# Optimization experiments

Measured on AMD Instinct MI355X. Metric: run time of the kernel, lower is better.

The kernel has to match this reference:

```python
import jax, jax.numpy as jnp
import numpy as np

H = 256      # hidden_dim
L = 3        # nb_layer
N = 10000    # nodes (shared between graph_1 and graph_2)
E1 = 131072  # edges in graph_1
E2 = 65536   # edges in graph_2
B = 16       # number of subgraphs / t_value batch


def _mlp(x, W0, b0, W1, b1, W2, b2):
    h = jax.nn.relu(x @ W0 + b0)
    h = jax.nn.relu(h @ W1 + b1)
    return h @ W2 + b2


def _gatv2(x, src, dst, e, Wl, bl, Wr, br, We, att, bias, n):
    # PyG GATv2Conv (heads=1): gather node features by edge, LeakyReLU attention
    # with edge encodings, scatter-softmax over destination nodes, scatter-add.
    xl = x @ Wl + bl                                            # (N, H)
    xr = x @ Wr + br                                            # (N, H)
    m = jax.nn.leaky_relu(xl[src] + xr[dst] + e @ We, 0.2)      # (E, H)
    logits = m @ att                                            # (E,)
    seg_max = jax.ops.segment_max(logits, dst, num_segments=n)
    ex = jnp.exp(logits - seg_max[dst])
    denom = jax.ops.segment_sum(ex, dst, num_segments=n)
    alpha = ex / (denom[dst] + 1e-16)                           # (E,)
    out = jax.ops.segment_sum(xl[src] * alpha[:, None], dst, num_segments=n)
    return out + bias


def _forward(edge_attr1, edge_attr2, t_value,
             te_W0, te_b0, te_W1, te_b1, te_W2, te_b2,
             ee_W0, ee_b0, ee_W1, ee_b1, ee_W2, ee_b2,
             dec_W0, dec_b0, dec_W1, dec_b1, dec_W2, dec_b2,
             gg_Wl, gg_bl, gg_Wr, gg_br, gg_We, gg_att, gg_bias,
             gf_Wl, gf_bl, gf_Wr, gf_br, gf_We, gf_att, gf_bias,
             edge_index1, edge_index2, batch):
    n = batch.shape[0]
    # time encoding per node, duplicated to 2H node features
    t_enc = _mlp(t_value[batch][:, None], te_W0, te_b0, te_W1, te_b1, te_W2, te_b2)  # (N, H)
    x = jnp.concatenate([t_enc, t_enc], axis=1)                                      # (N, 2H)
    e1 = _mlp(edge_attr1, ee_W0, ee_b0, ee_W1, ee_b1, ee_W2, ee_b2)                  # (E1, H)
    e2 = _mlp(edge_attr2[:, None], ee_W0, ee_b0, ee_W1, ee_b1, ee_W2, ee_b2)         # (E2, H)
    e1_init = e1
    src1, dst1 = edge_index1[0], edge_index1[1]
    src2, dst2 = edge_index2[0], edge_index2[1]
    for i in range(L):
        o1 = _gatv2(x, src1, dst1, e1, gg_Wl[i], gg_bl[i], gg_Wr[i], gg_br[i], gg_We[i], gg_att[i], gg_bias[i], n)
        o2 = _gatv2(x, src2, dst2, e2, gf_Wl[i], gf_bl[i], gf_Wr[i], gf_br[i], gf_We[i], gf_att[i], gf_bias[i], n)
        x = jnp.concatenate([o1, o2], axis=1)                                        # (N, 2H)
    # edge decoder: gather node pairs + initial edge encoding -> MLP
    dec_in = jnp.concatenate([x[src1], x[dst1], e1_init], axis=1)                    # (E1, 5H)
    return _mlp(dec_in, dec_W0, dec_b0, dec_W1, dec_b1, dec_W2, dec_b2)              # (E1, 1)


def setup_inputs() -> dict:
    ks = iter(jax.random.split(jax.random.key(0), 48))
    def nrm(shape, s=0.1):
        return jax.random.normal(next(ks), shape, dtype=jnp.float32) * s
    inp = {}
    inp["edge_index1"] = jax.random.randint(next(ks), (2, E1), 0, N)
    inp["edge_attr1"] = jax.random.uniform(next(ks), (E1, 1), dtype=jnp.float32)
    inp["edge_index2"] = jax.random.randint(next(ks), (2, E2), 0, N)
    inp["edge_attr2"] = jax.random.uniform(next(ks), (E2,), dtype=jnp.float32)
    inp["batch"] = jnp.sort(jax.random.randint(next(ks), (N,), 0, B))
    inp["t_value"] = jax.random.normal(next(ks), (B,), dtype=jnp.float32)
    for p in ["te", "ee"]:
        inp[p + "_W0"] = nrm((1, H)); inp[p + "_b0"] = jnp.zeros((H,), jnp.float32)
        inp[p + "_W1"] = nrm((H, H)); inp[p + "_b1"] = jnp.zeros((H,), jnp.float32)
        inp[p + "_W2"] = nrm((H, H)); inp[p + "_b2"] = jnp.zeros((H,), jnp.float32)
    inp["dec_W0"] = nrm((5 * H, H)); inp["dec_b0"] = jnp.zeros((H,), jnp.float32)
    inp["dec_W1"] = nrm((H, H));     inp["dec_b1"] = jnp.zeros((H,), jnp.float32)
    inp["dec_W2"] = nrm((H, 1));     inp["dec_b2"] = jnp.zeros((1,), jnp.float32)
    for p in ["gg", "gf"]:
        inp[p + "_Wl"] = nrm((L, 2 * H, H)); inp[p + "_bl"] = jnp.zeros((L, H), jnp.float32)
        inp[p + "_Wr"] = nrm((L, 2 * H, H)); inp[p + "_br"] = jnp.zeros((L, H), jnp.float32)
        inp[p + "_We"] = nrm((L, H, H))
        inp[p + "_att"] = nrm((L, H))
        inp[p + "_bias"] = jnp.zeros((L, H), jnp.float32)
    return inp


def reference(edge_index1, edge_attr1, edge_index2, edge_attr2, batch, t_value,
              te_W0, te_b0, te_W1, te_b1, te_W2, te_b2,
              ee_W0, ee_b0, ee_W1, ee_b1, ee_W2, ee_b2,
              dec_W0, dec_b0, dec_W1, dec_b1, dec_W2, dec_b2,
              gg_Wl, gg_bl, gg_Wr, gg_br, gg_We, gg_att, gg_bias,
              gf_Wl, gf_bl, gf_Wr, gf_br, gf_We, gf_att, gf_bias):
    return _forward(edge_attr1, edge_attr2, t_value,
                    te_W0, te_b0, te_W1, te_b1, te_W2, te_b2,
                    ee_W0, ee_b0, ee_W1, ee_b1, ee_W2, ee_b2,
                    dec_W0, dec_b0, dec_W1, dec_b1, dec_W2, dec_b2,
                    gg_Wl, gg_bl, gg_Wr, gg_br, gg_We, gg_att, gg_bias,
                    gf_Wl, gf_bl, gf_Wr, gf_br, gf_We, gf_att, gf_bias,
                    edge_index1, edge_index2, batch)
```

## Files before the change

kernel.cpp:

```cpp
#include <hip/hip_runtime.h>

#define Hd 256
#define NNODE 10000
#define NE1 131072
#define NE2 65536
#define TROWS 4097
#define TLD 1792

typedef __attribute__((ext_vector_type(8))) short bf16x8;
typedef __attribute__((ext_vector_type(4))) float f32x4;

#define MFMA16(a, b, c) __builtin_amdgcn_mfma_f32_16x16x32_bf16((a), (b), (c), 0, 0, 0)

__device__ __forceinline__ float b2f(ushort u) { return __uint_as_float(((unsigned)u) << 16); }
__device__ __forceinline__ ushort f2b(float f) {
  unsigned u = __float_as_uint(f);
  return (ushort)((u + 0x7fffu + ((u >> 16) & 1u)) >> 16);
}

__device__ __forceinline__ unsigned comb2(unsigned a, unsigned b, unsigned t) {
  float alo = __uint_as_float(a << 16), ahi = __uint_as_float(a & 0xffff0000u);
  float blo = __uint_as_float(b << 16), bhi = __uint_as_float(b & 0xffff0000u);
  float tlo = __uint_as_float(t << 16), thi = __uint_as_float(t & 0xffff0000u);
  float zlo = fmaxf(alo + blo + tlo, 0.f);
  float zhi = fmaxf(ahi + bhi + thi, 0.f);
  return ((unsigned)f2b(zhi) << 16) | (unsigned)f2b(zlo);
}


__global__ void time_mlp_k(const float* __restrict__ tval,
                           const float* __restrict__ W0, const float* __restrict__ b0,
                           const float* __restrict__ W1, const float* __restrict__ b1,
                           const float* __restrict__ W2, const float* __restrict__ b2,
                           float* __restrict__ tenc) {
  __shared__ float h0[Hd], h1[Hd];
  int b = blockIdx.x, j = threadIdx.x;
  float t = tval[b];
  h0[j] = fmaxf(t * W0[j] + b0[j], 0.f);
  __syncthreads();
  float a = b1[j];
  for (int k = 0; k < Hd; ++k) a += h0[k] * W1[k * Hd + j];
  h1[j] = fmaxf(a, 0.f);
  __syncthreads();
  float c = b2[j];
  for (int k = 0; k < Hd; ++k) c += h1[k] * W2[k * Hd + j];
  tenc[b * Hd + j] = c;
}

__global__ void build_x0_k(const int* __restrict__ batch, const float* __restrict__ tenc,
                           ushort* __restrict__ x0) {
  int idx = blockIdx.x * 256 + threadIdx.x;
  int n = idx >> 9;
  x0[idx] = f2b(tenc[batch[n] * Hd + (idx & 255)]);
}

__global__ void init_small_k(int* __restrict__ cnt1, int* __restrict__ cur1,
                             int* __restrict__ cnt2, int* __restrict__ cur2,
                             float* __restrict__ zerob, float* __restrict__ biascat,
                             const float* __restrict__ gg_bl, const float* __restrict__ gg_br,
                             const float* __restrict__ gf_bl, const float* __restrict__ gf_br) {
  int i = blockIdx.x * 256 + threadIdx.x;
  if (i < NNODE) { cnt1[i] = 0; cur1[i] = 0; cnt2[i] = 0; cur2[i] = 0; return; }
  i -= NNODE;
  if (i < 512) { zerob[i] = 0.f; return; }
  i -= 512;
  if (i < 6144) {
    int layer = i >> 10, c = i & 1023;
    float v;
    if (c < 256)      v = gg_bl[layer * 256 + c];
    else if (c < 512) v = gg_br[layer * 256 + c - 256];
    else if (c < 768) v = gf_bl[layer * 256 + c - 512];
    else              v = gf_br[layer * 256 + c - 768];
    biascat[layer * 1024 + c] = v;
  }
}

__global__ __launch_bounds__(256) void foldv2_k(
    const float* __restrict__ gg_We, const float* __restrict__ gf_We,
    const float* __restrict__ dec_W0, const float* __restrict__ eeW2,
    const float* __restrict__ eeb2,
    float* __restrict__ Wpart, float* __restrict__ bpart) {
  __shared__ float As[32][68];
  __shared__ float Bt[32][68];
  __shared__ float b2s[32];
  const int tid = threadIdx.x;
  const int bx = blockIdx.x, by = blockIdx.y, bz = blockIdx.z;
  const int y = bx >> 2, n0 = (bx & 3) * 64, k0 = by * 64;
  const int j0 = bz * 32;
  const bool by0 = (by == 0);
  const float* src;
  if (y < 6) src = ((y & 1) == 0 ? gg_We : gf_We) + (size_t)(y >> 1) * 65536;
  else       src = dec_W0 + 1024 * 256;
  if (tid < 32) b2s[tid] = eeb2[j0 + tid];
  {
    int nn = tid & 63, jj0 = tid >> 6;
#pragma unroll
    for (int p = 0; p < 8; ++p)
      As[jj0 + 4 * p][nn] = src[(size_t)(j0 + jj0 + 4 * p) * 256 + n0 + nn];
  }
  {
    int jj = tid & 31, kk0 = tid >> 5;
#pragma unroll
    for (int p = 0; p < 8; ++p)
      Bt[jj][kk0 + 8 * p] = eeW2[(size_t)(k0 + kk0 + 8 * p) * 256 + j0 + jj];
  }
  __syncthreads();
  const int tn = tid & 15, tk = tid >> 4;
  float acc[4][4];
#pragma unroll
  for (int a = 0; a < 4; ++a)
#pragma unroll
    for (int b = 0; b < 4; ++b) acc[a][b] = 0.f;
  float bacc[4] = {0.f, 0.f, 0.f, 0.f};
#pragma unroll 8
  for (int j = 0; j < 32; ++j) {
    float4 av = *(const float4*)&As[j][tn * 4];
    float4 bv = *(const float4*)&Bt[j][tk * 4];
    if (by0) {
      float eb = b2s[j];
      bacc[0] += eb * av.x; bacc[1] += eb * av.y;
      bacc[2] += eb * av.z; bacc[3] += eb * av.w;
    }
    acc[0][0] += av.x * bv.x; acc[0][1] += av.x * bv.y;
    acc[0][2] += av.x * bv.z; acc[0][3] += av.x * bv.w;
    acc[1][0] += av.y * bv.x; acc[1][1] += av.y * bv.y;
    acc[1][2] += av.y * bv.z; acc[1][3] += av.y * bv.w;
    acc[2][0] += av.z * bv.x; acc[2][1] += av.z * bv.y;
    acc[2][2] += av.z * bv.z; acc[2][3] += av.z * bv.w;
    acc[3][0] += av.w * bv.x; acc[3][1] += av.w * bv.y;
    acc[3][2] += av.w * bv.z; acc[3][3] += av.w * bv.w;
  }
  float* wp = Wpart + (size_t)bz * 458752;
#pragma unroll
  for (int a = 0; a < 4; ++a) {
    int n = n0 + tn * 4 + a;
#pragma unroll
    for (int b = 0; b < 4; ++b)
      wp[((size_t)y * 256 + n) * 256 + k0 + tk * 4 + b] = acc[a][b];
  }
  if (tk == 0 && by0) {
#pragma unroll
    for (int a = 0; a < 4; ++a)
      bpart[(size_t)bz * 1792 + y * 256 + n0 + tn * 4 + a] = bacc[a];
  }
}

__global__ __launch_bounds__(256) void foldr_k(
    const float* __restrict__ Wpart, const float* __restrict__ bpart,
    const float* __restrict__ dec_b0,
    ushort* __restrict__ WcatT, float* __restrict__ bcat) {
  int idx = blockIdx.x * 256 + threadIdx.x;
  float s = 0.f;
#pragma unroll
  for (int z = 0; z < 8; ++z) s += Wpart[(size_t)z * 458752 + idx];
  WcatT[idx] = f2b(s);
  if (idx < 1792) {
    float b = 0.f;
#pragma unroll
    for (int z = 0; z < 8; ++z) b += bpart[(size_t)z * 1792 + idx];
    if (idx >= 1536) b += dec_b0[idx - 1536];
    bcat[idx] = b;
  }
}

__global__ void build_h0_k(const float* __restrict__ W0, const float* __restrict__ b0,
                           ushort* __restrict__ h0b) {
  int i = blockIdx.x, j = threadIdx.x;
  float a = (float)i / 4096.f;
  h0b[(size_t)i * 256 + j] = f2b(fmaxf(a * W0[j] + b0[j], 0.f));
}

struct TT { const float* src; ushort* dst; int K; int n_off; int ld; int start; };
struct TransArgs { TT t[24]; };

__global__ void trans_all_k(TransArgs a) {
  int b = blockIdx.x;
  int ti = 0;
  while (ti + 1 < 24 && a.t[ti + 1].start <= b) ++ti;
  TT tk = a.t[ti];
  int lb = b - tk.start;
  int gx = tk.K >> 5;
  int k0 = (lb % gx) * 32, n0 = (lb / gx) * 32;
  __shared__ float t[32][33];
  int tx = threadIdx.x & 31, ty = threadIdx.x >> 5;
#pragma unroll
  for (int p = 0; p < 4; ++p)
    t[ty + 8 * p][tx] = tk.src[(size_t)(k0 + ty + 8 * p) * 256 + n0 + tx];
  __syncthreads();
#pragma unroll
  for (int p = 0; p < 4; ++p)
    tk.dst[(size_t)(tk.n_off + n0 + ty + 8 * p) * tk.ld + k0 + tx] = f2b(t[tx][ty + 8 * p]);
}


__global__ void deg_all_k(const int* __restrict__ dst1, int* __restrict__ cnt1,
                          const int* __restrict__ dst2, int* __restrict__ cnt2) {
  int e = blockIdx.x * 256 + threadIdx.x;
  if (e < NE1) atomicAdd(cnt1 + dst1[e], 1);
  else if (e - NE1 < NE2) atomicAdd(cnt2 + dst2[e - NE1], 1);
}

__global__ void scan_k(const int* __restrict__ cnt1, int* __restrict__ rs1,
                       const int* __restrict__ cnt2, int* __restrict__ rs2) {
  const int g = blockIdx.x;
  const int* cnt = g ? cnt2 : cnt1;
  int* rowstart = g ? rs2 : rs1;
  const int E = g ? NE2 : NE1;
  __shared__ int part[626];
  int t = threadIdx.x;
  if (t < 625) {
    int s = 0;
#pragma unroll
    for (int i = 0; i < 16; ++i) s += cnt[t * 16 + i];
    part[t] = s;
  }
  __syncthreads();
  if (t == 0) {
    int run = 0;
    for (int i = 0; i < 625; ++i) { int v = part[i]; part[i] = run; run += v; }
  }
  __syncthreads();
  if (t < 625) {
    int off = part[t];
#pragma unroll
    for (int i = 0; i < 16; ++i) { rowstart[t * 16 + i] = off; off += cnt[t * 16 + i]; }
  }
  if (t == 0) rowstart[NNODE] = E;
}

__global__ void fill_all_k(const int* __restrict__ dst1, const int* __restrict__ rs1,
                           int* __restrict__ cur1, int* __restrict__ eid1,
                           const int* __restrict__ src1, const float* __restrict__ eattr1,
                           int* __restrict__ srcs1, float* __restrict__ attrs1,
                           int* __restrict__ dsts1,
                           const int* __restrict__ dst2, const int* __restrict__ rs2,
                           int* __restrict__ cur2,
                           const int* __restrict__ src2, const float* __restrict__ eattr2,
                           int* __restrict__ srcs2, float* __restrict__ attrs2) {
  int e = blockIdx.x * 256 + threadIdx.x;
  if (e < NE1) {
    int d = dst1[e];
    int idx = rs1[d] + atomicAdd(cur1 + d, 1);
    eid1[idx] = e;
    srcs1[idx] = src1[e];
    attrs1[idx] = eattr1[e];
    dsts1[idx] = d;
  } else if (e - NE1 < NE2) {
    int e2 = e - NE1;
    int d = dst2[e2];
    int idx = rs2[d] + atomicAdd(cur2 + d, 1);
    srcs2[idx] = src2[e2];
    attrs2[idx] = eattr2[e2];
  }
}

__global__ __launch_bounds__(256) void attagg_k(
    const ushort* __restrict__ T, int tcol1, int tcol2,
    const float* __restrict__ att1, const float* __restrict__ att2,
    const ushort* __restrict__ xlr,
    const int* __restrict__ srcs1, const float* __restrict__ attrs1,
    const int* __restrict__ srcs2, const float* __restrict__ attrs2,
    const int* __restrict__ rs1, const int* __restrict__ rs2,
    const float* __restrict__ bias1, const float* __restrict__ bias2,
    ushort* __restrict__ xnext) {
  __shared__ float att_s[2][256], bias_s[2][256];
  __shared__ float acbuf[2][256];
  __shared__ float mden[2][2];
  const int tid = threadIdx.x;
  att_s[0][tid] = att1[tid];
  att_s[1][tid] = att2[tid];
  bias_s[0][tid] = bias1[tid];
  bias_s[1][tid] = bias2[tid];
  __syncthreads();
  const int wave = tid >> 6, lane = tid & 63;
  const int nloc = wave >> 1, sub = wave & 1;
  const bool g1 = blockIdx.x < (NNODE / 2);
  const int nid = (g1 ? blockIdx.x : blockIdx.x - NNODE / 2) * 2 + nloc;
  const int gi = g1 ? 0 : 1;
  const int* srcs = g1 ? srcs1 : srcs2;
  const float* attrs = g1 ? attrs1 : attrs2;
  const int* rowstart = g1 ? rs1 : rs2;
  const int goff = g1 ? 0 : 512;
  const int colbase = g1 ? 0 : 256;
  const ushort* Tg = T + (g1 ? tcol1 : tcol2);
  const int c = lane * 4;
  ushort4 xr4 = *(const ushort4*)(xlr + (size_t)nid * 1024 + goff + 256 + c);
  const float xr0 = b2f(xr4.x), xr1 = b2f(xr4.y), xr2 = b2f(xr4.z), xr3 = b2f(xr4.w);
  const float a0 = att_s[gi][c], a1 = att_s[gi][c + 1];
  const float a2 = att_s[gi][c + 2], a3 = att_s[gi][c + 3];
  const int s0 = rowstart[nid], s1 = rowstart[nid + 1];
  float m = -1e30f;
  float den = 0.f, ac0 = 0.f, ac1 = 0.f, ac2 = 0.f, ac3 = 0.f;
  {
    int i = s0 + sub;
    if (i < s1) {
      ushort4 xv0, lo0;
      ushort4 xv1 = {0, 0, 0, 0}, lo1 = {0, 0, 0, 0};
      {
        int s = srcs[i];
        int i0 = (int)(attrs[i] * 4096.f + 0.5f);
        i0 = i0 < 0 ? 0 : (i0 > 4096 ? 4096 : i0);
        lo0 = *(const ushort4*)(Tg + (size_t)i0 * TLD + c);
        xv0 = *(const ushort4*)(xlr + (size_t)s * 1024 + goff + c);
      }
      if (i + 2 < s1) {
        int s = srcs[i + 2];
        int i0 = (int)(attrs[i + 2] * 4096.f + 0.5f);
        i0 = i0 < 0 ? 0 : (i0 > 4096 ? 4096 : i0);
        lo1 = *(const ushort4*)(Tg + (size_t)i0 * TLD + c);
        xv1 = *(const ushort4*)(xlr + (size_t)s * 1024 + goff + c);
      }
      for (; i < s1; i += 2) {
        ushort4 xv_c = xv0, lo_c = lo0;
        xv0 = xv1; lo0 = lo1;
        if (i + 4 < s1) {
          int s = srcs[i + 4];
          int i0 = (int)(attrs[i + 4] * 4096.f + 0.5f);
          i0 = i0 < 0 ? 0 : (i0 > 4096 ? 4096 : i0);
          lo1 = *(const ushort4*)(Tg + (size_t)i0 * TLD + c);
          xv1 = *(const ushort4*)(xlr + (size_t)s * 1024 + goff + c);
        }
        float x0 = b2f(xv_c.x), x1 = b2f(xv_c.y), x2 = b2f(xv_c.z), x3 = b2f(xv_c.w);
        float z0 = x0 + xr0 + b2f(lo_c.x);
        float z1 = x1 + xr1 + b2f(lo_c.y);
        float z2 = x2 + xr2 + b2f(lo_c.z);
        float z3 = x3 + xr3 + b2f(lo_c.w);
        z0 = z0 > 0.f ? z0 : 0.2f * z0;
        z1 = z1 > 0.f ? z1 : 0.2f * z1;
        z2 = z2 > 0.f ? z2 : 0.2f * z2;
        z3 = z3 > 0.f ? z3 : 0.2f * z3;
        float p = z0 * a0 + z1 * a1 + z2 * a2 + z3 * a3;
#pragma unroll
        for (int dd = 1; dd < 64; dd <<= 1) p += __shfl_xor(p, dd);
        float mn = fmaxf(m, p);
        float sc = __expf(m - mn);
        float ww = __expf(p - mn);
        den = den * sc + ww;
        ac0 = ac0 * sc + ww * x0;
        ac1 = ac1 * sc + ww * x1;
        ac2 = ac2 * sc + ww * x2;
        ac3 = ac3 * sc + ww * x3;
        m = mn;
      }
    }
  }
  if (sub == 1) {
    acbuf[nloc][c + 0] = ac0;
    acbuf[nloc][c + 1] = ac1;
    acbuf[nloc][c + 2] = ac2;
    acbuf[nloc][c + 3] = ac3;
    if (lane == 0) { mden[nloc][0] = m; mden[nloc][1] = den; }
  }
  __syncthreads();
  if (sub == 0) {
    float m1 = mden[nloc][0], den1 = mden[nloc][1];
    float mn = fmaxf(m, m1);
    float sc0 = __expf(m - mn), sc1 = __expf(m1 - mn);
    float d = den * sc0 + den1 * sc1;
    float A0 = ac0 * sc0 + acbuf[nloc][c + 0] * sc1;
    float A1 = ac1 * sc0 + acbuf[nloc][c + 1] * sc1;
    float A2 = ac2 * sc0 + acbuf[nloc][c + 2] * sc1;
    float A3 = ac3 * sc0 + acbuf[nloc][c + 3] * sc1;
    float inv = 1.f / (d + 1e-16f);
    ushort4 o;
    o.x = f2b(A0 * inv + bias_s[gi][c + 0]);
    o.y = f2b(A1 * inv + bias_s[gi][c + 1]);
    o.z = f2b(A2 * inv + bias_s[gi][c + 2]);
    o.w = f2b(A3 * inv + bias_s[gi][c + 3]);
    *(ushort4*)(xnext + (size_t)nid * 512 + colbase + c) = o;
  }
}

template <bool RELU, bool OBF16>
__global__ __launch_bounds__(256, 2) void mgemm_k(
    const ushort* __restrict__ A, int lda, const ushort* __restrict__ WT, int K,
    const float* __restrict__ bias, void* __restrict__ C, int ldc, int M) {
  __shared__ ushort As[64][40];
  __shared__ ushort Bs[256][40];
  const int tid = threadIdx.x;
  const int wave = tid >> 6, lane = tid & 63;
  const int quad = lane >> 4, l15 = lane & 15;
  const int m0 = blockIdx.x * 64;
  const int ncol0 = blockIdx.y * 256;
  const ushort* WTb = WT + (size_t)ncol0 * K;
  const int arow = tid >> 2, akc = (tid & 3) << 3;
  int am = m0 + arow;
  if (am >= M) am = M - 1;
  f32x4 acc[4][4];
#pragma unroll
  for (int i = 0; i < 4; ++i)
#pragma unroll
    for (int j = 0; j < 4; ++j) acc[i][j] = (f32x4){0.f, 0.f, 0.f, 0.f};
  for (int k0 = 0; k0 < K; k0 += 32) {
    *(uint4*)&As[arow][akc] = *(const uint4*)(A + (size_t)am * lda + k0 + akc);
#pragma unroll
    for (int r = 0; r < 4; ++r) {
      int row = arow + r * 64;
      *(uint4*)&Bs[row][akc] = *(const uint4*)(WTb + (size_t)row * K + k0 + akc);
    }
    __syncthreads();
    bf16x8 bfr[4];
#pragma unroll
    for (int ni = 0; ni < 4; ++ni)
      bfr[ni] = *(const bf16x8*)&Bs[wave * 64 + ni * 16 + l15][quad * 8];
#pragma unroll
    for (int mi = 0; mi < 4; ++mi) {
      bf16x8 af = *(const bf16x8*)&As[mi * 16 + l15][quad * 8];
#pragma unroll
      for (int ni = 0; ni < 4; ++ni) acc[mi][ni] = MFMA16(af, bfr[ni], acc[mi][ni]);
    }
    __syncthreads();
  }
#pragma unroll
  for (int mi = 0; mi < 4; ++mi)
#pragma unroll
    for (int ni = 0; ni < 4; ++ni) {
      int c = ncol0 + wave * 64 + ni * 16 + l15;
      float bv = bias[c];
#pragma unroll
      for (int r = 0; r < 4; ++r) {
        int m = m0 + mi * 16 + quad * 4 + r;
        if (m < M) {
          float v = acc[mi][ni][r] + bv;
          if (RELU) v = fmaxf(v, 0.f);
          if (OBF16) ((ushort*)C)[(size_t)m * ldc + c] = f2b(v);
          else       ((float*)C)[(size_t)m * ldc + c] = v;
        }
      }
    }
}

__global__ __launch_bounds__(256, 4) void dec3_k(
    const float* __restrict__ attrs1, const ushort* __restrict__ T,
    const ushort* __restrict__ Z, const int* __restrict__ eid,
    const int* __restrict__ srcs1, const int* __restrict__ dsts1,
    const ushort* __restrict__ W1T, const float* __restrict__ b1,
    const float* __restrict__ W2, const float* __restrict__ b2,
    float* __restrict__ out) {
  __shared__ __align__(16) ushort h0[64][264];
  float* red = (float*)h0;
  const int tid = threadIdx.x;
  const int wave = tid >> 6, lane = tid & 63;
  const int quad = lane >> 4, l15 = lane & 15;
  const int m0 = blockIdx.x * 64;
  const int arow = tid >> 2;
  {
    int gs = srcs1[m0 + arow], gd = dsts1[m0 + arow];
    int i0 = (int)(attrs1[m0 + arow] * 4096.f + 0.5f);
    i0 = i0 < 0 ? 0 : (i0 > 4096 ? 4096 : i0);
    const int cq = (tid & 3) * 8;
    const ushort* za = Z + (size_t)gs * 512 + cq;
    const ushort* zb = Z + (size_t)gd * 512 + 256 + cq;
    const ushort* tz = T + (size_t)i0 * TLD + 1536 + cq;
    uint4 ra[8], rb[8], rt[8];
#pragma unroll
    for (int s = 0; s < 8; ++s) ra[s] = *(const uint4*)(za + 32 * s);
#pragma unroll
    for (int s = 0; s < 8; ++s) rb[s] = *(const uint4*)(zb + 32 * s);
#pragma unroll
    for (int s = 0; s < 8; ++s) rt[s] = *(const uint4*)(tz + 32 * s);
    __builtin_amdgcn_sched_barrier(0);
#pragma unroll
    for (int s = 0; s < 8; ++s) {
      uint4 o;
      o.x = comb2(ra[s].x, rb[s].x, rt[s].x);
      o.y = comb2(ra[s].y, rb[s].y, rt[s].y);
      o.z = comb2(ra[s].z, rb[s].z, rt[s].z);
      o.w = comb2(ra[s].w, rb[s].w, rt[s].w);
      *(uint4*)&h0[arow][cq + 32 * s] = o;
    }
  }
  __syncthreads();
  f32x4 acc2[4][4];
#pragma unroll
  for (int i = 0; i < 4; ++i)
#pragma unroll
    for (int j = 0; j < 4; ++j) acc2[i][j] = (f32x4){0.f, 0.f, 0.f, 0.f};
  for (int k0 = 0; k0 < 256; k0 += 32) {
    bf16x8 bfr[4];
#pragma unroll
    for (int ni = 0; ni < 4; ++ni)
      bfr[ni] = *(const bf16x8*)(W1T + (size_t)(wave * 64 + ni * 16 + l15) * 256 + k0 + quad * 8);
#pragma unroll
    for (int mi = 0; mi < 4; ++mi) {
      bf16x8 af = *(const bf16x8*)&h0[mi * 16 + l15][k0 + quad * 8];
#pragma unroll
      for (int ni = 0; ni < 4; ++ni) acc2[mi][ni] = MFMA16(af, bfr[ni], acc2[mi][ni]);
    }
  }
  float part[4][4];
#pragma unroll
  for (int mi = 0; mi < 4; ++mi)
#pragma unroll
    for (int r = 0; r < 4; ++r) part[mi][r] = 0.f;
#pragma unroll
  for (int mi = 0; mi < 4; ++mi)
#pragma unroll
    for (int ni = 0; ni < 4; ++ni) {
      int c = wave * 64 + ni * 16 + l15;
      float bv = b1[c], wv = W2[c];
#pragma unroll
      for (int r = 0; r < 4; ++r) {
        float v = fmaxf(acc2[mi][ni][r] + bv, 0.f);
        part[mi][r] += v * wv;
      }
    }
#pragma unroll
  for (int d = 1; d < 16; d <<= 1)
#pragma unroll
    for (int mi = 0; mi < 4; ++mi)
#pragma unroll
      for (int r = 0; r < 4; ++r) part[mi][r] += __shfl_xor(part[mi][r], d);
  __syncthreads();
  if (l15 == 0)
#pragma unroll
    for (int mi = 0; mi < 4; ++mi)
#pragma unroll
      for (int r = 0; r < 4; ++r) red[wave * 64 + mi * 16 + quad * 4 + r] = part[mi][r];
  __syncthreads();
  if (tid < 64) {
    float s = red[tid] + red[64 + tid] + red[128 + tid] + red[192 + tid];
    out[eid[m0 + tid]] = s + b2[0];
  }
}


extern "C" void kernel_launch(void* const* d_in, const int* in_sizes, int n_in,
                              void* d_out, int out_size, void* d_ws, size_t ws_size,
                              hipStream_t stream) {
  const int*   eidx1  = (const int*)d_in[0];
  const float* eattr1 = (const float*)d_in[1];
  const int*   eidx2  = (const int*)d_in[2];
  const float* eattr2 = (const float*)d_in[3];
  const int*   batch  = (const int*)d_in[4];
  const float* tval   = (const float*)d_in[5];
  const float* te_W0 = (const float*)d_in[6];
  const float* te_b0 = (const float*)d_in[7];
  const float* te_W1 = (const float*)d_in[8];
  const float* te_b1 = (const float*)d_in[9];
  const float* te_W2 = (const float*)d_in[10];
  const float* te_b2 = (const float*)d_in[11];
  const float* ee_W0 = (const float*)d_in[12];
  const float* ee_b0 = (const float*)d_in[13];
  const float* ee_W1 = (const float*)d_in[14];
  const float* ee_b1 = (const float*)d_in[15];
  const float* ee_W2 = (const float*)d_in[16];
  const float* ee_b2 = (const float*)d_in[17];
  const float* dec_W0 = (const float*)d_in[18];
  const float* dec_b0 = (const float*)d_in[19];
  const float* dec_W1 = (const float*)d_in[20];
  const float* dec_b1 = (const float*)d_in[21];
  const float* dec_W2 = (const float*)d_in[22];
  const float* dec_b2 = (const float*)d_in[23];
  const float* gg_Wl  = (const float*)d_in[24];
  const float* gg_bl  = (const float*)d_in[25];
  const float* gg_Wr  = (const float*)d_in[26];
  const float* gg_br  = (const float*)d_in[27];
  const float* gg_We  = (const float*)d_in[28];
  const float* gg_att = (const float*)d_in[29];
  const float* gg_bias= (const float*)d_in[30];
  const float* gf_Wl  = (const float*)d_in[31];
  const float* gf_bl  = (const float*)d_in[32];
  const float* gf_Wr  = (const float*)d_in[33];
  const float* gf_br  = (const float*)d_in[34];
  const float* gf_We  = (const float*)d_in[35];
  const float* gf_att = (const float*)d_in[36];
  const float* gf_bias= (const float*)d_in[37];
  (void)in_sizes; (void)n_in; (void)out_size; (void)ws_size;

  const int* src1 = eidx1;
  const int* dst1 = eidx1 + NE1;
  const int* src2 = eidx2;
  const int* dst2 = eidx2 + NE2;

  char* base = (char*)d_ws;
  size_t off = 0;
  auto alloc = [&](size_t bytes) {
    void* p = base + off;
    off += (bytes + 255) & ~(size_t)255;
    return p;
  };
  ushort* x_a    = (ushort*)alloc((size_t)NNODE * 512 * 2);
  ushort* x_b    = (ushort*)alloc((size_t)NNODE * 512 * 2);
  ushort* xlr    = (ushort*)alloc((size_t)NNODE * 1024 * 2);
  ushort* Z      = (ushort*)alloc((size_t)NNODE * 512 * 2);
  ushort* h0b    = (ushort*)alloc((size_t)TROWS * 256 * 2);
  ushort* H1     = (ushort*)alloc((size_t)TROWS * 256 * 2);
  ushort* T      = (ushort*)alloc((size_t)TROWS * TLD * 2);
  ushort* WcatT  = (ushort*)alloc((size_t)7 * 256 * 256 * 2);
  float*  bcat   = (float*)alloc((size_t)TLD * 4);
  float*  tenc   = (float*)alloc((size_t)16 * Hd * 4);
  ushort* decZT  = (ushort*)alloc((size_t)512 * 512 * 2);
  ushort* decW1T = (ushort*)alloc((size_t)256 * 256 * 2);
  ushort* eeW1T  = (ushort*)alloc((size_t)256 * 256 * 2);
  ushort* wlrT   = (ushort*)alloc((size_t)6 * 512 * 512 * 2);
  float*  biascat= (float*)alloc((size_t)6 * 1024 * 4);
  float*  zerob  = (float*)alloc((size_t)512 * 4);
  int* cnt1      = (int*)alloc((size_t)NNODE * 4);
  int* cur1      = (int*)alloc((size_t)NNODE * 4);
  int* rs1       = (int*)alloc((size_t)(NNODE + 1) * 4);
  int* eid1      = (int*)alloc((size_t)NE1 * 4);
  int* srcs1     = (int*)alloc((size_t)NE1 * 4);
  float* attrs1  = (float*)alloc((size_t)NE1 * 4);
  int* dsts1     = (int*)alloc((size_t)NE1 * 4);
  int* cnt2      = (int*)alloc((size_t)NNODE * 4);
  int* cur2      = (int*)alloc((size_t)NNODE * 4);
  int* rs2       = (int*)alloc((size_t)(NNODE + 1) * 4);
  int* srcs2     = (int*)alloc((size_t)NE2 * 4);
  float* attrs2  = (float*)alloc((size_t)NE2 * 4);

  float* Wpart = (float*)T;
  float* bpart = (float*)H1;

  float* out = (float*)d_out;

  init_small_k<<<(NNODE + 512 + 6144 + 255) / 256, 256, 0, stream>>>(
      cnt1, cur1, cnt2, cur2, zerob, biascat, gg_bl, gg_br, gf_bl, gf_br);
  foldv2_k<<<dim3(28, 4, 8), 256, 0, stream>>>(gg_We, gf_We, dec_W0, ee_W2, ee_b2,
                                               Wpart, bpart);
  foldr_k<<<1792, 256, 0, stream>>>(Wpart, bpart, dec_b0, WcatT, bcat);
  build_h0_k<<<TROWS, 256, 0, stream>>>(ee_W0, ee_b0, h0b);

  TransArgs ta;
  int nt = 0, cum = 0;
  auto add = [&](const float* s, ushort* d, int K, int noff, int ld) {
    ta.t[nt].src = s; ta.t[nt].dst = d; ta.t[nt].K = K;
    ta.t[nt].n_off = noff; ta.t[nt].ld = ld; ta.t[nt].start = cum;
    cum += (K / 32) * 8; ++nt;
  };
  add(dec_W1, decW1T, 256, 0, 256);
  add(ee_W1, eeW1T, 256, 0, 256);
  add(dec_W0, decZT, 512, 0, 512);
  add(dec_W0 + 512 * 256, decZT, 512, 256, 512);
  for (int i = 0; i < 3; ++i) {
    add(gg_Wl + (size_t)i * 512 * 256, wlrT + (size_t)(2 * i) * 512 * 512, 512, 0, 512);
    add(gg_Wr + (size_t)i * 512 * 256, wlrT + (size_t)(2 * i) * 512 * 512, 512, 256, 512);
    add(gf_Wl + (size_t)i * 512 * 256, wlrT + (size_t)(2 * i + 1) * 512 * 512, 512, 0, 512);
    add(gf_Wr + (size_t)i * 512 * 256, wlrT + (size_t)(2 * i + 1) * 512 * 512, 512, 256, 512);
  }
  for (int i = nt; i < 24; ++i) ta.t[i].start = 0x7fffffff;
  trans_all_k<<<cum, 256, 0, stream>>>(ta);

  mgemm_k<true, true><<<dim3((TROWS + 63) / 64, 1), 256, 0, stream>>>(
      h0b, 256, eeW1T, 256, ee_b1, H1, 256, TROWS);
  mgemm_k<false, true><<<dim3((TROWS + 63) / 64, 7), 256, 0, stream>>>(
      H1, 256, WcatT, 256, bcat, T, TLD, TROWS);

  deg_all_k<<<(NE1 + NE2) / 256, 256, 0, stream>>>(dst1, cnt1, dst2, cnt2);
  scan_k<<<2, 640, 0, stream>>>(cnt1, rs1, cnt2, rs2);
  fill_all_k<<<(NE1 + NE2) / 256, 256, 0, stream>>>(
      dst1, rs1, cur1, eid1, src1, eattr1, srcs1, attrs1, dsts1,
      dst2, rs2, cur2, src2, eattr2, srcs2, attrs2);

  time_mlp_k<<<16, 256, 0, stream>>>(tval, te_W0, te_b0, te_W1, te_b1, te_W2, te_b2, tenc);
  build_x0_k<<<(NNODE * 512) / 256, 256, 0, stream>>>(batch, tenc, x_a);

  ushort* x_cur = x_a;
  ushort* x_nxt = x_b;
  const int ngrid = (NNODE + 63) / 64;
  for (int i = 0; i < 3; ++i) {
    mgemm_k<false, true><<<dim3(ngrid, 4), 256, 0, stream>>>(
        x_cur, 512, wlrT + (size_t)(2 * i) * 512 * 512, 512, biascat + (size_t)i * 1024, xlr, 1024, NNODE);
    attagg_k<<<NNODE, 256, 0, stream>>>(
        T, (2 * i) * 256, (2 * i + 1) * 256,
        gg_att + i * Hd, gf_att + i * Hd, xlr,
        srcs1, attrs1, srcs2, attrs2, rs1, rs2,
        gg_bias + i * Hd, gf_bias + i * Hd, x_nxt);
    ushort* t = x_cur; x_cur = x_nxt; x_nxt = t;
  }

  mgemm_k<false, true><<<dim3(ngrid, 2), 256, 0, stream>>>(
      x_cur, 512, decZT, 512, zerob, Z, 512, NNODE);
  dec3_k<<<NE1 / 64, 256, 0, stream>>>(attrs1, T, Z, eid1, srcs1, dsts1,
                                       decW1T, dec_b1, dec_W2, dec_b2, out);
}
```

Measured before the change: 503.7 us.

## Batch edge attention four-wide and software-pipeline GEMM tile loads

The GATv2 aggregation loop now handles four edges per iteration per half-wave. It prefetches the next four gathers and batches the shuffle reductions, so a single online-softmax rescale covers four edges instead of one. The generic GEMM moves to K-step 64 with register prefetch of the next tile while MFMAs run on the current one, plus a launch-bounds hint of 3 blocks per CU. The edge-MLP second layer double-buffers its global weight fragments. The costs are higher register pressure, which may spill under the tighter launch bound, and clamped duplicate loads at segment tails.

```diff
diff --git a/kernel.cpp b/kernel.cpp
--- a/kernel.cpp
+++ b/kernel.cpp
@@ -294,52 +294,60 @@
   {
     int i = s0 + sub;
     if (i < s1) {
-      ushort4 xv0, lo0;
-      ushort4 xv1 = {0, 0, 0, 0}, lo1 = {0, 0, 0, 0};
-      {
-        int s = srcs[i];
-        int i0 = (int)(attrs[i] * 4096.f + 0.5f);
-        i0 = i0 < 0 ? 0 : (i0 > 4096 ? 4096 : i0);
-        lo0 = *(const ushort4*)(Tg + (size_t)i0 * TLD + c);
-        xv0 = *(const ushort4*)(xlr + (size_t)s * 1024 + goff + c);
-      }
-      if (i + 2 < s1) {
-        int s = srcs[i + 2];
-        int i0 = (int)(attrs[i + 2] * 4096.f + 0.5f);
-        i0 = i0 < 0 ? 0 : (i0 > 4096 ? 4096 : i0);
-        lo1 = *(const ushort4*)(Tg + (size_t)i0 * TLD + c);
-        xv1 = *(const ushort4*)(xlr + (size_t)s * 1024 + goff + c);
-      }
-      for (; i < s1; i += 2) {
-        ushort4 xv_c = xv0, lo_c = lo0;
-        xv0 = xv1; lo0 = lo1;
-        if (i + 4 < s1) {
-          int s = srcs[i + 4];
-          int i0 = (int)(attrs[i + 4] * 4096.f + 0.5f);
+      ushort4 xv[4], lo[4];
+      auto LDB = [&](int base, ushort4* xvp, ushort4* lop) {
+#pragma unroll
+        for (int e = 0; e < 4; ++e) {
+          int idx = base + 2 * e;
+          idx = idx < s1 ? idx : (s1 - 1);
+          int s = srcs[idx];
+          int i0 = (int)(attrs[idx] * 4096.f + 0.5f);
           i0 = i0 < 0 ? 0 : (i0 > 4096 ? 4096 : i0);
-          lo1 = *(const ushort4*)(Tg + (size_t)i0 * TLD + c);
-          xv1 = *(const ushort4*)(xlr + (size_t)s * 1024 + goff + c);
+          lop[e] = *(const ushort4*)(Tg + (size_t)i0 * TLD + c);
+          xvp[e] = *(const ushort4*)(xlr + (size_t)s * 1024 + goff + c);
         }
-        float x0 = b2f(xv_c.x), x1 = b2f(xv_c.y), x2 = b2f(xv_c.z), x3 = b2f(xv_c.w);
-        float z0 = x0 + xr0 + b2f(lo_c.x);
-        float z1 = x1 + xr1 + b2f(lo_c.y);
-        float z2 = x2 + xr2 + b2f(lo_c.z);
-        float z3 = x3 + xr3 + b2f(lo_c.w);
-        z0 = z0 > 0.f ? z0 : 0.2f * z0;
-        z1 = z1 > 0.f ? z1 : 0.2f * z1;
-        z2 = z2 > 0.f ? z2 : 0.2f * z2;
-        z3 = z3 > 0.f ? z3 : 0.2f * z3;
-        float p = z0 * a0 + z1 * a1 + z2 * a2 + z3 * a3;
-#pragma unroll
-        for (int dd = 1; dd < 64; dd <<= 1) p += __shfl_xor(p, dd);
-        float mn = fmaxf(m, p);
+      };
+      LDB(i, xv, lo);
+      for (; i < s1; i += 8) {
+        ushort4 xc[4], lc[4];
+#pragma unroll
+        for (int e = 0; e < 4; ++e) { xc[e] = xv[e]; lc[e] = lo[e]; }
+        if (i + 8 < s1) LDB(i + 8, xv, lo);
+        float pe[4], xs[4][4];
+#pragma unroll
+        for (int e = 0; e < 4; ++e) {
+          float x0 = b2f(xc[e].x), x1 = b2f(xc[e].y), x2 = b2f(xc[e].z), x3 = b2f(xc[e].w);
+          xs[e][0] = x0; xs[e][1] = x1; xs[e][2] = x2; xs[e][3] = x3;
+          float z0 = x0 + xr0 + b2f(lc[e].x);
+          float z1 = x1 + xr1 + b2f(lc[e].y);
+          float z2 = x2 + xr2 + b2f(lc[e].z);
+          float z3 = x3 + xr3 + b2f(lc[e].w);
+          z0 = z0 > 0.f ? z0 : 0.2f * z0;
+          z1 = z1 > 0.f ? z1 : 0.2f * z1;
+          z2 = z2 > 0.f ? z2 : 0.2f * z2;
+          z3 = z3 > 0.f ? z3 : 0.2f * z3;
+          pe[e] = z0 * a0 + z1 * a1 + z2 * a2 + z3 * a3;
+        }
+#pragma unroll
+        for (int dd = 1; dd < 64; dd <<= 1) {
+          pe[0] += __shfl_xor(pe[0], dd);
+          pe[1] += __shfl_xor(pe[1], dd);
+          pe[2] += __shfl_xor(pe[2], dd);
+          pe[3] += __shfl_xor(pe[3], dd);
+        }
+        pe[1] = (i + 2 < s1) ? pe[1] : -1e30f;
+        pe[2] = (i + 4 < s1) ? pe[2] : -1e30f;
+        pe[3] = (i + 6 < s1) ? pe[3] : -1e30f;
+        float mn = fmaxf(fmaxf(m, pe[0]), fmaxf(pe[1], pe[2]));
+        mn = fmaxf(mn, pe[3]);
         float sc = __expf(m - mn);
-        float ww = __expf(p - mn);
-        den = den * sc + ww;
-        ac0 = ac0 * sc + ww * x0;
-        ac1 = ac1 * sc + ww * x1;
-        ac2 = ac2 * sc + ww * x2;
-        ac3 = ac3 * sc + ww * x3;
+        float w0 = __expf(pe[0] - mn), w1 = __expf(pe[1] - mn);
+        float w2 = __expf(pe[2] - mn), w3 = __expf(pe[3] - mn);
+        den = den * sc + ((w0 + w1) + (w2 + w3));
+        ac0 = ac0 * sc + (w0 * xs[0][0] + w1 * xs[1][0]) + (w2 * xs[2][0] + w3 * xs[3][0]);
+        ac1 = ac1 * sc + (w0 * xs[0][1] + w1 * xs[1][1]) + (w2 * xs[2][1] + w3 * xs[3][1]);
+        ac2 = ac2 * sc + (w0 * xs[0][2] + w1 * xs[1][2]) + (w2 * xs[2][2] + w3 * xs[3][2]);
+        ac3 = ac3 * sc + (w0 * xs[0][3] + w1 * xs[1][3]) + (w2 * xs[2][3] + w3 * xs[3][3]);
         m = mn;
       }
     }
@@ -372,11 +380,11 @@
 }
 
 template <bool RELU, bool OBF16>
-__global__ __launch_bounds__(256, 2) void mgemm_k(
+__global__ __launch_bounds__(256, 3) void mgemm_k(
     const ushort* __restrict__ A, int lda, const ushort* __restrict__ WT, int K,
     const float* __restrict__ bias, void* __restrict__ C, int ldc, int M) {
-  __shared__ ushort As[64][40];
-  __shared__ ushort Bs[256][40];
+  __shared__ ushort As[64][72];
+  __shared__ ushort Bs[256][72];
   const int tid = threadIdx.x;
   const int wave = tid >> 6, lane = tid & 63;
   const int quad = lane >> 4, l15 = lane & 15;
@@ -386,29 +394,53 @@
   const int arow = tid >> 2, akc = (tid & 3) << 3;
   int am = m0 + arow;
   if (am >= M) am = M - 1;
+  const ushort* Arow = A + (size_t)am * lda;
+  const ushort* Brow = WTb + (size_t)arow * K;
   f32x4 acc[4][4];
 #pragma unroll
   for (int i = 0; i < 4; ++i)
 #pragma unroll
     for (int j = 0; j < 4; ++j) acc[i][j] = (f32x4){0.f, 0.f, 0.f, 0.f};
-  for (int k0 = 0; k0 < K; k0 += 32) {
-    *(uint4*)&As[arow][akc] = *(const uint4*)(A + (size_t)am * lda + k0 + akc);
-#pragma unroll
-    for (int r = 0; r < 4; ++r) {
-      int row = arow + r * 64;
-      *(uint4*)&Bs[row][akc] = *(const uint4*)(WTb + (size_t)row * K + k0 + akc);
+  uint4 pf[10];
+  auto LDT = [&](int k0) {
+    pf[0] = *(const uint4*)(Arow + k0 + akc);
+    pf[1] = *(const uint4*)(Arow + k0 + 32 + akc);
+#pragma unroll
+    for (int rr = 0; rr < 4; ++rr) {
+      pf[2 + 2 * rr] = *(const uint4*)(Brow + (size_t)(rr * 64) * K + k0 + akc);
+      pf[3 + 2 * rr] = *(const uint4*)(Brow + (size_t)(rr * 64) * K + k0 + 32 + akc);
+    }
+  };
+  auto STT = [&]() {
+    *(uint4*)&As[arow][akc] = pf[0];
+    *(uint4*)&As[arow][32 + akc] = pf[1];
+#pragma unroll
+    for (int rr = 0; rr < 4; ++rr) {
+      *(uint4*)&Bs[arow + rr * 64][akc] = pf[2 + 2 * rr];
+      *(uint4*)&Bs[arow + rr * 64][32 + akc] = pf[3 + 2 * rr];
+    }
+  };
+  LDT(0);
+  STT();
+  __syncthreads();
+  for (int k0 = 0; k0 < K; k0 += 64) {
+    const bool more = (k0 + 64 < K);
+    if (more) LDT(k0 + 64);
+#pragma unroll
+    for (int kk = 0; kk < 64; kk += 32) {
+      bf16x8 bfr[4];
+#pragma unroll
+      for (int ni = 0; ni < 4; ++ni)
+        bfr[ni] = *(const bf16x8*)&Bs[wave * 64 + ni * 16 + l15][kk + quad * 8];
+#pragma unroll
+      for (int mi = 0; mi < 4; ++mi) {
+        bf16x8 af = *(const bf16x8*)&As[mi * 16 + l15][kk + quad * 8];
+#pragma unroll
+        for (int ni = 0; ni < 4; ++ni) acc[mi][ni] = MFMA16(af, bfr[ni], acc[mi][ni]);
+      }
     }
     __syncthreads();
-    bf16x8 bfr[4];
-#pragma unroll
-    for (int ni = 0; ni < 4; ++ni)
-      bfr[ni] = *(const bf16x8*)&Bs[wave * 64 + ni * 16 + l15][quad * 8];
-#pragma unroll
-    for (int mi = 0; mi < 4; ++mi) {
-      bf16x8 af = *(const bf16x8*)&As[mi * 16 + l15][quad * 8];
-#pragma unroll
-      for (int ni = 0; ni < 4; ++ni) acc[mi][ni] = MFMA16(af, bfr[ni], acc[mi][ni]);
-    }
+    if (more) STT();
     __syncthreads();
   }
 #pragma unroll
@@ -476,17 +508,26 @@
   for (int i = 0; i < 4; ++i)
 #pragma unroll
     for (int j = 0; j < 4; ++j) acc2[i][j] = (f32x4){0.f, 0.f, 0.f, 0.f};
+  const ushort* wb = W1T + (size_t)(wave * 64 + l15) * 256 + quad * 8;
+  bf16x8 bcur[4], bnxt[4];
+#pragma unroll
+  for (int ni = 0; ni < 4; ++ni)
+    bcur[ni] = *(const bf16x8*)(wb + (size_t)(ni * 16) * 256);
+#pragma unroll
   for (int k0 = 0; k0 < 256; k0 += 32) {
-    bf16x8 bfr[4];
-#pragma unroll
-    for (int ni = 0; ni < 4; ++ni)
-      bfr[ni] = *(const bf16x8*)(W1T + (size_t)(wave * 64 + ni * 16 + l15) * 256 + k0 + quad * 8);
+    if (k0 + 32 < 256) {
+#pragma unroll
+      for (int ni = 0; ni < 4; ++ni)
+        bnxt[ni] = *(const bf16x8*)(wb + (size_t)(ni * 16) * 256 + k0 + 32);
+    }
 #pragma unroll
     for (int mi = 0; mi < 4; ++mi) {
       bf16x8 af = *(const bf16x8*)&h0[mi * 16 + l15][k0 + quad * 8];
 #pragma unroll
-      for (int ni = 0; ni < 4; ++ni) acc2[mi][ni] = MFMA16(af, bfr[ni], acc2[mi][ni]);
-    }
+      for (int ni = 0; ni < 4; ++ni) acc2[mi][ni] = MFMA16(af, bcur[ni], acc2[mi][ni]);
+    }
+#pragma unroll
+    for (int ni = 0; ni < 4; ++ni) bcur[ni] = bnxt[ni];
   }
   float part[4][4];
 #pragma unroll
```

Result: slower. 710.4 us (+41.0%).
